# Optimization experiments

Hardware: AMD Instinct MI355X
Metric: run time of the kernel (lower is better)

The kernel has to match this reference:

```python
import jax, jax.numpy as jnp
import numpy as np

HEADS = 16
DIM_HEAD = 64

def setup_inputs() -> dict:
    key = jax.random.key(0)
    ks = jax.random.split(key, 5)
    B, S, D = 2, 2048, 1024
    return {
        "hidden_states": jax.random.normal(ks[0], (B, S, D), dtype=jnp.float32),
        "Wq": jax.random.normal(ks[1], (D, D), dtype=jnp.float32) * (D ** -0.5),
        "Wkv": jax.random.normal(ks[2], (D, D), dtype=jnp.float32) * (D ** -0.5),
        "Wout": jax.random.normal(ks[3], (D, D), dtype=jnp.float32) * (D ** -0.5),
        "bout": jnp.zeros((D,), dtype=jnp.float32),
    }

def reference(hidden_states, Wq, Wkv, Wout, bout):
    B, S, D = hidden_states.shape
    H, Dh = HEADS, DIM_HEAD
    # projections (torch Linear: x @ W.T; here weights are stored as [in, out])
    q = hidden_states @ Wq            # [B, S, D]
    kv = hidden_states @ Wkv          # key == value share the to_kv projection
    q = q.reshape(B, S, H, Dh).transpose(0, 2, 1, 3)   # [B, H, S, Dh]
    k = kv.reshape(B, S, H, Dh).transpose(0, 2, 1, 3)
    v = k
    scale = 1.0 / np.sqrt(Dh).astype(np.float32)
    # ReLU attention: no softmax
    attn = jax.nn.relu(jnp.einsum("bhsd,bhtd->bhst", q, k) * scale)  # [B,H,S,S]
    out = jnp.einsum("bhst,bhtd->bhsd", attn, v)                     # [B,H,S,Dh]
    out = out.transpose(0, 2, 1, 3).reshape(B, S, H * Dh)
    return out @ Wout + bout
```

## Files before the change

kernel.cpp:

```cpp
#include <hip/hip_runtime.h>
#include <hip/hip_bf16.h>

#define HEADS  16
#define DIMH   64
#define NBATCH 2
#define SEQ    2048
#define DMODEL 1024
#define MROWS  (NBATCH * SEQ)

typedef __attribute__((ext_vector_type(8)))  short bf16x8;
typedef __attribute__((ext_vector_type(4)))  float f32x4;
typedef __attribute__((ext_vector_type(16))) float f32x16;
typedef __attribute__((ext_vector_type(4)))  float float4v;
typedef __attribute__((ext_vector_type(4)))  short short4v;

__device__ inline void glds16(const void* g, void* l) {
    __builtin_amdgcn_global_load_lds(
        (const __attribute__((address_space(1))) unsigned int*)g,
        (__attribute__((address_space(3))) unsigned int*)l, 16, 0, 0);
}

#define WAIT_VMCNT(N) asm volatile("s_waitcnt vmcnt(" #N ")" ::: "memory")
#define BARRIER() do { __builtin_amdgcn_s_barrier(); asm volatile("" ::: "memory"); } while (0)

__global__ void cvt_kernel(const float* __restrict__ in,
                           __hip_bfloat16* __restrict__ out, int n4) {
    int i = blockIdx.x * blockDim.x + threadIdx.x;
    if (i >= n4) return;
    float4v v = reinterpret_cast<const float4v*>(in)[i];
    union { short4v s; __hip_bfloat16 h[4]; } u;
#pragma unroll
    for (int j = 0; j < 4; ++j) u.h[j] = __float2bfloat16(v[j]);
    reinterpret_cast<short4v*>(out)[i] = u.s;
}

__global__ void tr_kernel(const float* __restrict__ W,
                          __hip_bfloat16* __restrict__ WT) {
    __shared__ float tile[32][33];
    int i = blockIdx.y * 32 + threadIdx.y;
    int o = blockIdx.x * 32 + threadIdx.x;
    tile[threadIdx.y][threadIdx.x] = W[i * DMODEL + o];
    __syncthreads();
    int oo = blockIdx.x * 32 + threadIdx.y;
    int ii = blockIdx.y * 32 + threadIdx.x;
    WT[oo * DMODEL + ii] = __float2bfloat16(tile[threadIdx.x][threadIdx.y]);
}


__launch_bounds__(512, 2)
__global__ void proj_kernel(const __hip_bfloat16* __restrict__ hsb,
                            const __hip_bfloat16* __restrict__ WqT,
                            const __hip_bfloat16* __restrict__ WkvT,
                            __hip_bfloat16* __restrict__ qb,
                            __hip_bfloat16* __restrict__ kb,
                            __hip_bfloat16* __restrict__ vtb) {
    __shared__ __align__(16) char SLDS[73728];
    char (*Alds)[8192]  = (char (*)[8192])SLDS;
    char (*Blds)[16384] = (char (*)[16384])(SLDS + 24576);
    char* CT = SLDS;

    const int tid  = threadIdx.x;
    const int wave = tid >> 6;
    const int lane = tid & 63;
    const int lr = lane & 15;
    const int lk = lane >> 4;
    const int wm = wave >> 2, wn = wave & 3;

    int bid = blockIdx.x;
    bid = (bid & 7) * 32 + (bid >> 3);
    const int xt = bid & 7;
    const int mt = bid >> 3;
    const bool is_q = xt < 4;
    const int mbase = mt * 128;
    const int nbase = (xt & 3) * 256;
    const __hip_bfloat16* __restrict__ WT = is_q ? WqT : WkvT;

    const char* __restrict__ Ab = (const char*)(hsb + (size_t)mbase * DMODEL);
    const char* __restrict__ Bb = (const char*)(WT + (size_t)nbase * DMODEL);

    auto stage = [&](int buf, int k0) {
        const size_t colb = (size_t)k0 * 2 + lk * 16;
        glds16(Ab + (size_t)(wave * 16 + lr) * (DMODEL * 2) + colb,
               &Alds[buf][wave * 1024]);
#pragma unroll
        for (int r = 0; r < 2; ++r)
            glds16(Bb + (size_t)((r * 8 + wave) * 16 + lr) * (DMODEL * 2) + colb,
                   &Blds[buf][r * 8192 + wave * 1024]);
    };

    stage(0, 0);
    stage(1, 32);

    f32x4 acc[4][4] = {};
    int c0 = 0;
    for (int t = 0; t < DMODEL / 32; ++t) {
        if (t < DMODEL / 32 - 1) WAIT_VMCNT(3); else WAIT_VMCNT(0);
        BARRIER();
        if (t + 2 < DMODEL / 32) {
            int sb = c0 + 2; if (sb >= 3) sb -= 3;
            stage(sb, (t + 2) * 32);
        }
        bf16x8 af[4], bfr[4];
#pragma unroll
        for (int i = 0; i < 4; ++i) {
            af[i]  = *reinterpret_cast<const bf16x8*>(&Alds[c0][(wm * 4 + i) * 1024 + lane * 16]);
            bfr[i] = *reinterpret_cast<const bf16x8*>(&Blds[c0][(wn * 4 + i) * 1024 + lane * 16]);
        }
#pragma unroll
        for (int i = 0; i < 4; ++i)
#pragma unroll
            for (int j = 0; j < 4; ++j)
                acc[i][j] = __builtin_amdgcn_mfma_f32_16x16x32_bf16(af[i], bfr[j], acc[i][j], 0, 0, 0);
        c0 = (c0 + 1 == 3) ? 0 : c0 + 1;
    }

    const float qscale = is_q ? 0.125f : 1.0f;
    const int b_ = mbase >> 11;
    const int s0 = mbase & (SEQ - 1);
    BARRIER();

#pragma unroll
    for (int i = 0; i < 4; ++i)
#pragma unroll
        for (int j = 0; j < 4; ++j)
#pragma unroll
            for (int r = 0; r < 4; ++r) {
                int m = wm * 64 + i * 16 + lk * 4 + r;
                int n = wn * 64 + j * 16 + lr;
                *reinterpret_cast<__hip_bfloat16*>(
                    &CT[m * 512 + ((n * 2) ^ (((m >> 2) & 7) << 4))]) =
                    __float2bfloat16(acc[i][j][r] * qscale);
            }
    BARRIER();

    __hip_bfloat16* __restrict__ dst0 = is_q ? qb : kb;
#pragma unroll
    for (int p = 0; p < 8; ++p) {
        int g = p * 64 + (tid >> 3);
        int m = g >> 2, seg = g & 3, o = tid & 7;
        int key = ((m >> 2) & 7) << 4;
        bf16x8 val = *reinterpret_cast<const bf16x8*>(
            &CT[m * 512 + ((seg * 128 + o * 16) ^ key)]);
        int h = (nbase >> 6) + seg;
        *reinterpret_cast<bf16x8*>(
            &dst0[(((size_t)b_ * HEADS + h) * SEQ + s0 + m) * DIMH + o * 8]) = val;
    }

    if (!is_q) {
        BARRIER();
#pragma unroll
        for (int i = 0; i < 4; ++i)
#pragma unroll
            for (int j = 0; j < 4; ++j)
#pragma unroll
                for (int r = 0; r < 4; ++r) {
                    int m = wm * 64 + i * 16 + lk * 4 + r;
                    int n = wn * 64 + j * 16 + lr;
                    *reinterpret_cast<__hip_bfloat16*>(
                        &CT[n * 256 + ((m * 2) ^ ((n & 7) << 4))]) =
                        __float2bfloat16(acc[i][j][r]);
                }
        BARRIER();
#pragma unroll
        for (int p = 0; p < 8; ++p) {
            int g = p * 64 + (tid >> 3);
            int n = g >> 1, half = g & 1, o = tid & 7;
            int key2 = (n & 7) << 4;
            bf16x8 val = *reinterpret_cast<const bf16x8*>(
                &CT[n * 256 + ((half * 128 + o * 16) ^ key2)]);
            int h = (nbase >> 6) + (n >> 6);
            int dh = n & 63;
            *reinterpret_cast<bf16x8*>(
                &vtb[(((size_t)b_ * HEADS + h) * DIMH + dh) * SEQ + s0 + half * 64 + o * 8]) = val;
        }
    }
}

__launch_bounds__(512, 2)
__global__ void outproj_kernel(const __hip_bfloat16* __restrict__ ao,
                               const __hip_bfloat16* __restrict__ WoT,
                               const float* __restrict__ bout,
                               float* __restrict__ out) {
    __shared__ __align__(16) char Alds[3][8192];
    __shared__ __align__(16) char Blds[3][8192];
    const int tid  = threadIdx.x;
    const int wave = tid >> 6;
    const int lane = tid & 63;
    const int lr = lane & 15;
    const int lk = lane >> 4;
    const int wm = wave >> 1, wn = wave & 1;

    int bid = blockIdx.x;
    bid = (bid & 7) * 32 + (bid >> 3);
    const int xt = bid & 7;
    const int mt = bid >> 3;
    const int mbase = mt * 128;
    const int nbase = xt * 128;

    const char* __restrict__ Ab = (const char*)(ao + (size_t)mbase * DMODEL);
    const char* __restrict__ Bb = (const char*)(WoT + (size_t)nbase * DMODEL);

    auto stage = [&](int buf, int k0) {
        const size_t colb = (size_t)k0 * 2 + lk * 16;
        glds16(Ab + (size_t)(wave * 16 + lr) * (DMODEL * 2) + colb,
               &Alds[buf][wave * 1024]);
        glds16(Bb + (size_t)(wave * 16 + lr) * (DMODEL * 2) + colb,
               &Blds[buf][wave * 1024]);
    };

    stage(0, 0);
    stage(1, 32);

    f32x4 acc[2][4] = {};
    int c0 = 0;
    for (int t = 0; t < DMODEL / 32; ++t) {
        if (t < DMODEL / 32 - 1) WAIT_VMCNT(2); else WAIT_VMCNT(0);
        BARRIER();
        if (t + 2 < DMODEL / 32) {
            int sb = c0 + 2; if (sb >= 3) sb -= 3;
            stage(sb, (t + 2) * 32);
        }
        bf16x8 af[2], bfr[4];
#pragma unroll
        for (int i = 0; i < 2; ++i)
            af[i] = *reinterpret_cast<const bf16x8*>(&Alds[c0][(wm * 2 + i) * 1024 + lane * 16]);
#pragma unroll
        for (int j = 0; j < 4; ++j)
            bfr[j] = *reinterpret_cast<const bf16x8*>(&Blds[c0][(wn * 4 + j) * 1024 + lane * 16]);
#pragma unroll
        for (int i = 0; i < 2; ++i)
#pragma unroll
            for (int j = 0; j < 4; ++j)
                acc[i][j] = __builtin_amdgcn_mfma_f32_16x16x32_bf16(af[i], bfr[j], acc[i][j], 0, 0, 0);
        c0 = (c0 + 1 == 3) ? 0 : c0 + 1;
    }

#pragma unroll
    for (int j = 0; j < 4; ++j) {
        const int n = nbase + wn * 64 + j * 16 + lr;
        const float bias = bout[n];
#pragma unroll
        for (int i = 0; i < 2; ++i) {
#pragma unroll
            for (int r = 0; r < 4; ++r) {
                int m = mbase + wm * 32 + i * 16 + lk * 4 + r;
                out[(size_t)m * DMODEL + n] = acc[i][j][r] + bias;
            }
        }
    }
}

__launch_bounds__(256, 2)
__global__ void attn_kernel(const __hip_bfloat16* __restrict__ qb,
                            const __hip_bfloat16* __restrict__ kb,
                            const __hip_bfloat16* __restrict__ vtb,
                            __hip_bfloat16* __restrict__ ao) {
    __shared__ __align__(16) char Klds[4][8192];
    __shared__ __align__(16) char Vlds[4][8192];
    const int lane = threadIdx.x & 63;
    const int wave = threadIdx.x >> 6;
    const int l32  = lane & 31;
    const int hi   = lane >> 5;

    int bid = blockIdx.x;
    bid = (bid & 7) * 64 + (bid >> 3);
    const int bh   = bid >> 4;
    const int qblk = bid & 15;
    const int b_ = bh >> 4, h = bh & 15;
    const int qbase = qblk * 128 + wave * 32;

    const __hip_bfloat16* __restrict__ Q = qb + (size_t)bh * SEQ * DIMH;
    const char* __restrict__ Kg = (const char*)(kb  + (size_t)bh * SEQ * DIMH);
    const char* __restrict__ Vg = (const char*)(vtb + (size_t)bh * DIMH * SEQ);

    bf16x8 qf[4];
#pragma unroll
    for (int ks = 0; ks < 4; ++ks)
        qf[ks] = *reinterpret_cast<const bf16x8*>(
            &Q[(size_t)(qbase + l32) * DIMH + ks * 16 + hi * 8]);

    auto stage = [&](int buf, int t0) {
#pragma unroll
        for (int pass = 0; pass < 2; ++pass) {
            const int b   = wave * 2048 + pass * 1024 + lane * 16;
            const int row = b >> 7;
            const int cb  = (b & 127) ^ ((row & 7) << 4);
            glds16(Kg + (size_t)(t0 + row) * 128 + cb,
                   &Klds[buf][wave * 2048 + pass * 1024]);
            glds16(Vg + (size_t)row * (SEQ * 2) + t0 * 2 + cb,
                   &Vlds[buf][wave * 2048 + pass * 1024]);
        }
    };

    const int swz = (l32 & 7) << 4;
    f32x16 acco[2] = {};
    f32x16 sp0, sp1;

    auto do_qk = [&](const char* Kc) {
        sp0 = f32x16{}; sp1 = f32x16{};
        __builtin_amdgcn_s_setprio(1);
#pragma unroll
        for (int ks = 0; ks < 4; ++ks) {
            bf16x8 k0f = *reinterpret_cast<const bf16x8*>(
                Kc + l32 * 128        + ((ks * 32 + 16 * hi) ^ swz));
            bf16x8 k1f = *reinterpret_cast<const bf16x8*>(
                Kc + (32 + l32) * 128 + ((ks * 32 + 16 * hi) ^ swz));
            sp0 = __builtin_amdgcn_mfma_f32_32x32x16_bf16(k0f, qf[ks], sp0, 0, 0, 0);
            sp1 = __builtin_amdgcn_mfma_f32_32x32x16_bf16(k1f, qf[ks], sp1, 0, 0, 0);
        }
        __builtin_amdgcn_s_setprio(0);
    };

    auto do_packpv = [&](const char* Vc) {
        __builtin_amdgcn_s_setprio(1);
#pragma unroll
        for (int kt = 0; kt < 4; ++kt) {
            union { __hip_bfloat16 hh[8]; bf16x8 v; } pa;
            const int rb = (kt & 1) * 8;
#pragma unroll
            for (int j = 0; j < 8; ++j) {
                float x = (kt < 2) ? sp0[rb + j] : sp1[rb + j];
                pa.hh[j] = __float2bfloat16(fmaxf(x, 0.f));
            }
#pragma unroll
            for (int nt = 0; nt < 2; ++nt) {
                const int row = nt * 32 + l32;
                union { unsigned long long d[2]; bf16x8 v; } vb;
                vb.d[0] = *reinterpret_cast<const unsigned long long*>(
                    Vc + row * 128 + ((kt * 32 + 8 * hi) ^ swz));
                vb.d[1] = *reinterpret_cast<const unsigned long long*>(
                    Vc + row * 128 + ((kt * 32 + 16 + 8 * hi) ^ swz));
                acco[nt] = __builtin_amdgcn_mfma_f32_32x32x16_bf16(pa.v, vb.v, acco[nt], 0, 0, 0);
            }
        }
        __builtin_amdgcn_s_setprio(0);
    };

    stage(0, 0);
    stage(1, 64);

    WAIT_VMCNT(4);
    BARRIER();
    stage(2, 128);
    do_qk(Klds[0]);

    for (int t = 1; t < SEQ / 64; ++t) {
        if (t < SEQ / 64 - 1) WAIT_VMCNT(4); else WAIT_VMCNT(0);
        BARRIER();
        if (t + 2 < SEQ / 64) stage((t + 2) & 3, (t + 2) * 64);
        do_packpv(Vlds[(t - 1) & 3]);
        do_qk(Klds[t & 3]);
    }
    do_packpv(Vlds[(SEQ / 64 - 1) & 3]);

#pragma unroll
    for (int nt = 0; nt < 2; ++nt) {
#pragma unroll
        for (int r = 0; r < 16; ++r) {
            int q = qbase + (r & 3) + 8 * (r >> 2) + 4 * hi;
            ao[(size_t)(b_ * SEQ + q) * DMODEL + h * 64 + nt * 32 + l32] =
                __float2bfloat16(acco[nt][r]);
        }
    }
}

extern "C" void kernel_launch(void* const* d_in, const int* in_sizes, int n_in,
                              void* d_out, int out_size, void* d_ws, size_t ws_size,
                              hipStream_t stream) {
    const float* hs   = (const float*)d_in[0];
    const float* Wq   = (const float*)d_in[1];
    const float* Wkv  = (const float*)d_in[2];
    const float* Wout = (const float*)d_in[3];
    const float* bout = (const float*)d_in[4];
    float* out = (float*)d_out;

    char* ws = (char*)d_ws;
    size_t off = 0;
    auto alloc = [&](size_t bytes) { char* p = ws + off; off += bytes; return p; };
    __hip_bfloat16* hsb  = (__hip_bfloat16*)alloc((size_t)MROWS * DMODEL * 2);
    __hip_bfloat16* WqT  = (__hip_bfloat16*)alloc((size_t)DMODEL * DMODEL * 2);
    __hip_bfloat16* WkvT = (__hip_bfloat16*)alloc((size_t)DMODEL * DMODEL * 2);
    __hip_bfloat16* WoT  = (__hip_bfloat16*)alloc((size_t)DMODEL * DMODEL * 2);
    __hip_bfloat16* qb   = (__hip_bfloat16*)alloc((size_t)MROWS * DMODEL * 2);
    __hip_bfloat16* kb   = (__hip_bfloat16*)alloc((size_t)MROWS * DMODEL * 2);
    __hip_bfloat16* vtb  = (__hip_bfloat16*)alloc((size_t)MROWS * DMODEL * 2);
    __hip_bfloat16* ao   = hsb;

    cvt_kernel<<<(MROWS * DMODEL / 4 + 255) / 256, 256, 0, stream>>>(hs, hsb, MROWS * DMODEL / 4);
    dim3 trg(32, 32), trb(32, 32);
    tr_kernel<<<trg, trb, 0, stream>>>(Wq, WqT);
    tr_kernel<<<trg, trb, 0, stream>>>(Wkv, WkvT);
    tr_kernel<<<trg, trb, 0, stream>>>(Wout, WoT);

    proj_kernel<<<256, 512, 0, stream>>>(hsb, WqT, WkvT, qb, kb, vtb);

    attn_kernel<<<NBATCH * HEADS * (SEQ / 128), 256, 0, stream>>>(qb, kb, vtb, ao);

    outproj_kernel<<<256, 512, 0, stream>>>(ao, WoT, bout, out);
}
```

Baseline: 118.1 us.

## Stage K/V tiles into LDS in MFMA fragment order for contiguous reads

The attention kernel now loads K and V tiles into LDS already arranged in per-lane MFMA operand order. Each lane then reads its fragment as one contiguous 16-byte LDS load, where before it used swizzled row-major addressing and two 8-byte loads for V. To keep PV operands contiguous, the V-transpose producer permutes the element order it writes into the vtb buffer. This trades simpler, wider LDS reads and no XOR math for global loads that touch 32-byte segments per row, which may hurt coalescing.

Result: slower. 120.6 us (+2.2%).

```diff
diff --git a/kernel.cpp b/kernel.cpp
--- a/kernel.cpp
+++ b/kernel.cpp
@@ -166,12 +166,17 @@
             int g = p * 64 + (tid >> 3);
             int n = g >> 1, half = g & 1, o = tid & 7;
             int key2 = (n & 7) << 4;
-            bf16x8 val = *reinterpret_cast<const bf16x8*>(
-                &CT[n * 256 + ((half * 128 + o * 16) ^ key2)]);
+            int D = half * 64 + o * 8;
+            int mm = D >> 4, H = o & 1;
+            union { unsigned long long d[2]; bf16x8 v; } val;
+            val.d[0] = *reinterpret_cast<const unsigned long long*>(
+                &CT[n * 256 + ((mm * 32 + H * 8) ^ key2)]);
+            val.d[1] = *reinterpret_cast<const unsigned long long*>(
+                &CT[n * 256 + ((mm * 32 + 16 + H * 8) ^ key2)]);
             int h = (nbase >> 6) + (n >> 6);
             int dh = n & 63;
             *reinterpret_cast<bf16x8*>(
-                &vtb[(((size_t)b_ * HEADS + h) * DIMH + dh) * SEQ + s0 + half * 64 + o * 8]) = val;
+                &vtb[(((size_t)b_ * HEADS + h) * DIMH + dh) * SEQ + s0 + D]) = val.v;
         }
     }
 }
@@ -281,18 +286,17 @@
 
     auto stage = [&](int buf, int t0) {
 #pragma unroll
-        for (int pass = 0; pass < 2; ++pass) {
-            const int b   = wave * 2048 + pass * 1024 + lane * 16;
-            const int row = b >> 7;
-            const int cb  = (b & 127) ^ ((row & 7) << 4);
-            glds16(Kg + (size_t)(t0 + row) * 128 + cb,
-                   &Klds[buf][wave * 2048 + pass * 1024]);
-            glds16(Vg + (size_t)row * (SEQ * 2) + t0 * 2 + cb,
-                   &Vlds[buf][wave * 2048 + pass * 1024]);
-        }
-    };
-
-    const int swz = (l32 & 7) << 4;
+        for (int p = 0; p < 2; ++p) {
+            glds16(Kg + (size_t)(t0 + p * 32 + (lane & 31)) * 128 +
+                       wave * 32 + (lane >> 5) * 16,
+                   &Klds[buf][(p * 4 + wave) * 1024]);
+            const int rv = p * 4 + wave;
+            glds16(Vg + (size_t)((rv & 1) * 32 + (lane & 31)) * (SEQ * 2) +
+                       (size_t)(t0 + (rv >> 1) * 16) * 2 + (lane >> 5) * 16,
+                   &Vlds[buf][rv * 1024]);
+        }
+    };
+
     f32x16 acco[2] = {};
     f32x16 sp0, sp1;
 
@@ -301,10 +305,8 @@
         __builtin_amdgcn_s_setprio(1);
 #pragma unroll
         for (int ks = 0; ks < 4; ++ks) {
-            bf16x8 k0f = *reinterpret_cast<const bf16x8*>(
-                Kc + l32 * 128        + ((ks * 32 + 16 * hi) ^ swz));
-            bf16x8 k1f = *reinterpret_cast<const bf16x8*>(
-                Kc + (32 + l32) * 128 + ((ks * 32 + 16 * hi) ^ swz));
+            bf16x8 k0f = *reinterpret_cast<const bf16x8*>(Kc + ks * 1024 + lane * 16);
+            bf16x8 k1f = *reinterpret_cast<const bf16x8*>(Kc + (4 + ks) * 1024 + lane * 16);
             sp0 = __builtin_amdgcn_mfma_f32_32x32x16_bf16(k0f, qf[ks], sp0, 0, 0, 0);
             sp1 = __builtin_amdgcn_mfma_f32_32x32x16_bf16(k1f, qf[ks], sp1, 0, 0, 0);
         }
@@ -324,13 +326,9 @@
             }
 #pragma unroll
             for (int nt = 0; nt < 2; ++nt) {
-                const int row = nt * 32 + l32;
-                union { unsigned long long d[2]; bf16x8 v; } vb;
-                vb.d[0] = *reinterpret_cast<const unsigned long long*>(
-                    Vc + row * 128 + ((kt * 32 + 8 * hi) ^ swz));
-                vb.d[1] = *reinterpret_cast<const unsigned long long*>(
-                    Vc + row * 128 + ((kt * 32 + 16 + 8 * hi) ^ swz));
-                acco[nt] = __builtin_amdgcn_mfma_f32_32x32x16_bf16(pa.v, vb.v, acco[nt], 0, 0, 0);
+                bf16x8 vbv = *reinterpret_cast<const bf16x8*>(
+                    Vc + (kt * 2 + nt) * 1024 + lane * 16);
+                acco[nt] = __builtin_amdgcn_mfma_f32_32x32x16_bf16(pa.v, vbv, acco[nt], 0, 0, 0);
             }
         }
         __builtin_amdgcn_s_setprio(0);
```
